# Performance work log

Hardware: AMD Instinct MI355X
Metric: run time of the kernel (lower is better)

The kernel has to match this reference:

```python
import jax, jax.numpy as jnp
import numpy as np

EPS = 1e-20
SCALE = 1.0 / np.sqrt(128.0).astype(np.float32)


def setup_inputs() -> dict:
    key = jax.random.key(0)
    k1, k2 = jax.random.split(key)
    B, K, J, I = 64, 16, 512, 128
    inputs = jax.random.normal(k1, (B, J, I), dtype=jnp.float32)
    W = jax.random.normal(k2, (K, J, I), dtype=jnp.float32)
    b = jnp.zeros((K, J, 1), dtype=jnp.float32)
    return {"inputs": inputs, "W": W, "b": b}


def _squash(s):
    # squash(v) = (1 - 1/(exp(||v||)+eps)) * v / (||v|| + eps), norm over last dim
    n = jnp.linalg.norm(s, axis=-1, keepdims=True)
    return (1.0 - 1.0 / (jnp.exp(n) + EPS)) * (s / (n + EPS))


def reference(inputs, W, b):
    # inputs: (B, J, I); W: (K, J, I); b: (K, J, 1)
    u = inputs[..., None, :, :] * W            # (B, K, J, I) broadcast multiply
    c = jnp.sum(u * u, axis=-1, keepdims=True) * SCALE  # (B, K, J, 1)
    c = jax.nn.softmax(c, axis=0)              # softmax over BATCH dim, as in source
    c = c + b                                  # bias broadcast over batch
    s = jnp.sum(u * c, axis=-2)                # (B, K, I) weighted sum over in_channel
    return _squash(s)
```

## Files before the change

### kernel.cpp

```cpp
#include <hip/hip_runtime.h>
#include <math.h>

#define B 64
#define K 16
#define J 512
#define I 128
#define SCALE 0.08838834764831845f
#define EPSF 1e-20f

typedef __attribute__((ext_vector_type(8))) short short8;
typedef __attribute__((ext_vector_type(4))) float f32x4;

static __device__ __forceinline__ unsigned f2bf(float f) {
    union { float f; unsigned u; } v; v.f = f;
    return (v.u + 0x7FFFu + ((v.u >> 16) & 1u)) >> 16;
}

__global__ __launch_bounds__(64) void k1_mfma(const float* __restrict__ x,
                                              const float* __restrict__ w,
                                              const float* __restrict__ bias,
                                              float* __restrict__ cw) {
    __shared__ __align__(16) char lx[64 * 256];
    __shared__ __align__(16) char lw[16 * 256];

    const int j = blockIdx.x;
    const int l = threadIdx.x;
    const int q = l & 31, hi = l >> 5;

    const float4* xs = (const float4*)x;
    const float4* wsrc = (const float4*)w;

#pragma unroll
    for (int it = 0; it < 32; ++it) {
        int b = it * 2 + hi;
        float4 v = xs[((size_t)b * J + j) * 32 + q];
        uint2 u;
        u.x = f2bf(v.x * v.x) | (f2bf(v.y * v.y) << 16);
        u.y = f2bf(v.z * v.z) | (f2bf(v.w * v.w) << 16);
        *(uint2*)(lx + b * 256 + ((q * 8) ^ ((b & 7) << 4))) = u;
    }
#pragma unroll
    for (int it = 0; it < 8; ++it) {
        int k = it * 2 + hi;
        float4 v = wsrc[((size_t)k * J + j) * 32 + q];
        uint2 u;
        u.x = f2bf(v.x * v.x) | (f2bf(v.y * v.y) << 16);
        u.y = f2bf(v.z * v.z) | (f2bf(v.w * v.w) << 16);
        *(uint2*)(lw + k * 256 + ((q * 8) ^ ((k & 7) << 4))) = u;
    }
    __syncthreads();

    const int g = l >> 4, n = l & 15;
    f32x4 acc[4];
#pragma unroll
    for (int t = 0; t < 4; ++t) acc[t] = (f32x4){0.f, 0.f, 0.f, 0.f};

#pragma unroll
    for (int s = 0; s < 4; ++s) {
        const int colb = s * 64 + g * 16;
        short8 af = *(const short8*)(lw + n * 256 + (colb ^ ((n & 7) << 4)));
#pragma unroll
        for (int t = 0; t < 4; ++t) {
            int row = t * 16 + n;
            short8 bf = *(const short8*)(lx + row * 256 + (colb ^ ((row & 7) << 4)));
            acc[t] = __builtin_amdgcn_mfma_f32_16x16x32_bf16(af, bf, acc[t], 0, 0, 0);
        }
    }

    float sc[4][4];
#pragma unroll
    for (int t = 0; t < 4; ++t)
#pragma unroll
        for (int r = 0; r < 4; ++r) sc[t][r] = acc[t][r] * SCALE;

#pragma unroll
    for (int r = 0; r < 4; ++r) {
        float mx = fmaxf(fmaxf(sc[0][r], sc[1][r]), fmaxf(sc[2][r], sc[3][r]));
#pragma unroll
        for (int msk = 1; msk <= 8; msk <<= 1) mx = fmaxf(mx, __shfl_xor(mx, msk, 64));
        float e0 = expf(sc[0][r] - mx), e1 = expf(sc[1][r] - mx);
        float e2 = expf(sc[2][r] - mx), e3 = expf(sc[3][r] - mx);
        float sum = e0 + e1 + e2 + e3;
#pragma unroll
        for (int msk = 1; msk <= 8; msk <<= 1) sum += __shfl_xor(sum, msk, 64);
        float inv = 1.f / sum;
        int m = g * 4 + r;
        float bi = bias[m * J + j];
        size_t base = ((size_t)m * J + j) * B + n;
        cw[base]      = e0 * inv + bi;
        cw[base + 16] = e1 * inv + bi;
        cw[base + 32] = e2 * inv + bi;
        cw[base + 48] = e3 * inv + bi;
    }
}

__global__ __launch_bounds__(256) void k3_wsum(
    const float* __restrict__ x, const float* __restrict__ w,
    const float* __restrict__ cw, float* __restrict__ sp, int Jc) {
    __shared__ float cl[128 * 16];
    __shared__ float red[256 * 36];

    const int nwg = gridDim.x;
    const int raw = blockIdx.x;
    const int cpx = nwg >> 3;
    const int swz = (raw & 7) * cpx + (raw >> 3);
    const int kt = swz & 3;
    const int bt = (swz >> 2) & 15;
    const int jh = swz >> 6;
    const int j0 = jh * Jc;
    const int b0 = bt * 4, k0 = kt * 4;

    const int iq = threadIdx.x & 31;
    const int js = threadIdx.x >> 5;

    for (int idx = threadIdx.x; idx < Jc * 16; idx += 256) {
        int jj = idx >> 4, kk = (idx >> 2) & 3, bb = idx & 3;
        cl[idx] = cw[((size_t)(k0 + kk) * J + j0 + jj) * B + b0 + bb];
    }
    __syncthreads();

    float4 acc[4][4];
#pragma unroll
    for (int bb = 0; bb < 4; ++bb)
#pragma unroll
        for (int kk = 0; kk < 4; ++kk) acc[bb][kk] = make_float4(0.f, 0.f, 0.f, 0.f);

    for (int j = j0 + js; j < j0 + Jc; j += 8) {
        float4 xv[4], wv[4];
#pragma unroll
        for (int bb = 0; bb < 4; ++bb)
            xv[bb] = *(const float4*)(x + ((size_t)(b0 + bb) * J + j) * I + iq * 4);
#pragma unroll
        for (int kk = 0; kk < 4; ++kk)
            wv[kk] = *(const float4*)(w + ((size_t)(k0 + kk) * J + j) * I + iq * 4);
        const float* cj = cl + (j - j0) * 16;
#pragma unroll
        for (int kk = 0; kk < 4; ++kk) {
#pragma unroll
            for (int bb = 0; bb < 4; ++bb) {
                float c = cj[kk * 4 + bb];
                acc[bb][kk].x = fmaf(xv[bb].x * wv[kk].x, c, acc[bb][kk].x);
                acc[bb][kk].y = fmaf(xv[bb].y * wv[kk].y, c, acc[bb][kk].y);
                acc[bb][kk].z = fmaf(xv[bb].z * wv[kk].z, c, acc[bb][kk].z);
                acc[bb][kk].w = fmaf(xv[bb].w * wv[kk].w, c, acc[bb][kk].w);
            }
        }
    }

#pragma unroll
    for (int r = 0; r < 2; ++r) {
        __syncthreads();
#pragma unroll
        for (int s = 0; s < 8; ++s) {
            int slot = r * 8 + s;
            int bb = slot >> 2, kk = slot & 3;
            *(float4*)(red + (js * 32 + iq) * 36 + s * 4) = acc[bb][kk];
        }
        __syncthreads();
        int iq2 = threadIdx.x & 31, s2 = threadIdx.x >> 5;
        float4 v = make_float4(0.f, 0.f, 0.f, 0.f);
#pragma unroll
        for (int jss = 0; jss < 8; ++jss) {
            float4 u = *(const float4*)(red + (jss * 32 + iq2) * 36 + s2 * 4);
            v.x += u.x; v.y += u.y; v.z += u.z; v.w += u.w;
        }
        int slot = r * 8 + s2;
        int bb = slot >> 2, kk = slot & 3;
        *(float4*)(sp + (((size_t)jh * B + b0 + bb) * K + k0 + kk) * I + iq2 * 4) = v;
    }
}

__global__ __launch_bounds__(128) void k4_squash(const float* __restrict__ sp,
                                                 float* __restrict__ out, int nparts) {
    const int bk = blockIdx.x;
    const int i = threadIdx.x;
    const size_t stride = (size_t)B * K * I;
    const size_t base = (size_t)bk * I + i;

    float s = 0.f;
    for (int p = 0; p < nparts; ++p) s += sp[base + p * stride];

    float q = s * s;
#pragma unroll
    for (int m = 32; m >= 1; m >>= 1) q += __shfl_xor(q, m, 64);
    __shared__ float red2[2];
    if ((threadIdx.x & 63) == 0) red2[threadIdx.x >> 6] = q;
    __syncthreads();
    float nsq = red2[0] + red2[1];

    float n = sqrtf(nsq);
    float factor = (1.0f - 1.0f / (expf(n) + EPSF)) / (n + EPSF);
    out[base] = s * factor;
}

extern "C" void kernel_launch(void* const* d_in, const int* in_sizes, int n_in,
                              void* d_out, int out_size, void* d_ws, size_t ws_size,
                              hipStream_t stream) {
    const float* x    = (const float*)d_in[0];
    const float* w    = (const float*)d_in[1];
    const float* bias = (const float*)d_in[2];
    float* out = (float*)d_out;

    const size_t cwf   = (size_t)K * J * B;
    const size_t partf = (size_t)B * K * I;

    int jc = 16;
    if (ws_size < (cwf + 16 * partf) * 4) jc = 8;
    if (ws_size < (cwf + 8 * partf) * 4)  jc = 4;
    const int Jc = J / jc;

    float* cw = (float*)d_ws;
    float* sp = cw + cwf;

    hipLaunchKernelGGL(k1_mfma,  dim3(J),       dim3(64),  0, stream, x, w, bias, cw);
    hipLaunchKernelGGL(k3_wsum,  dim3(64 * jc), dim3(256), 0, stream, x, w, cw, sp, Jc);
    hipLaunchKernelGGL(k4_squash, dim3(B * K),  dim3(128), 0, stream, sp, out, jc);
}
```

Baseline: 29.84 us.

## Retile capsule kernels: wider k1 loads, tiled weight layout, fixed J split, lighter reductions

```diff
diff --git a/kernel.cpp b/kernel.cpp
--- a/kernel.cpp
+++ b/kernel.cpp
@@ -7,6 +7,8 @@
 #define I 128
 #define SCALE 0.08838834764831845f
 #define EPSF 1e-20f
+#define JC 8
+#define JCW 64
 
 typedef __attribute__((ext_vector_type(8))) short short8;
 typedef __attribute__((ext_vector_type(4))) float f32x4;
@@ -16,41 +18,42 @@
     return (v.u + 0x7FFFu + ((v.u >> 16) & 1u)) >> 16;
 }
 
-__global__ __launch_bounds__(64) void k1_mfma(const float* __restrict__ x,
-                                              const float* __restrict__ w,
-                                              const float* __restrict__ bias,
-                                              float* __restrict__ cw) {
-    __shared__ __align__(16) char lx[64 * 256];
-    __shared__ __align__(16) char lw[16 * 256];
-
-    const int j = blockIdx.x;
-    const int l = threadIdx.x;
-    const int q = l & 31, hi = l >> 5;
-
-    const float4* xs = (const float4*)x;
-    const float4* wsrc = (const float4*)w;
-
-#pragma unroll
-    for (int it = 0; it < 32; ++it) {
-        int b = it * 2 + hi;
-        float4 v = xs[((size_t)b * J + j) * 32 + q];
+__global__ __launch_bounds__(256) void k1_mfma(const float* __restrict__ x,
+                                               const float* __restrict__ w,
+                                               const float* __restrict__ bias,
+                                               float* __restrict__ cw2) {
+    __shared__ __align__(16) char lds[80 * 256];
+    char* lx = lds;
+    char* lw = lds + 64 * 256;
+
+    const int raw = blockIdx.x;
+    const int j = (raw & 7) * JCW + (raw >> 3);
+    const int tid = threadIdx.x;
+
+#pragma unroll
+    for (int r = 0; r < 8; ++r) {
+        int item = tid + 256 * r;
+        int row = item >> 5, q = item & 31;
+        float4 v = *(const float4*)(x + ((size_t)row * J + j) * I + q * 4);
         uint2 u;
         u.x = f2bf(v.x * v.x) | (f2bf(v.y * v.y) << 16);
         u.y = f2bf(v.z * v.z) | (f2bf(v.w * v.w) << 16);
-        *(uint2*)(lx + b * 256 + ((q * 8) ^ ((b & 7) << 4))) = u;
-    }
-#pragma unroll
-    for (int it = 0; it < 8; ++it) {
-        int k = it * 2 + hi;
-        float4 v = wsrc[((size_t)k * J + j) * 32 + q];
+        *(uint2*)(lx + row * 256 + ((q * 8) ^ ((row & 7) << 4))) = u;
+    }
+#pragma unroll
+    for (int r = 0; r < 2; ++r) {
+        int item = tid + 256 * r;
+        int k = item >> 5, q = item & 31;
+        float4 v = *(const float4*)(w + ((size_t)k * J + j) * I + q * 4);
         uint2 u;
         u.x = f2bf(v.x * v.x) | (f2bf(v.y * v.y) << 16);
         u.y = f2bf(v.z * v.z) | (f2bf(v.w * v.w) << 16);
-        *(uint2*)(lw + k * 256 + ((q * 8) ^ ((k & 7) << 4))) = u;
+        *(uint2*)(lw + k * 256 + ((k & 7) ? ((q * 8) ^ ((k & 7) << 4)) : q * 8)) = u;
     }
     __syncthreads();
-
-    const int g = l >> 4, n = l & 15;
+    if (tid >= 64) return;
+
+    const int g = tid >> 4, n = tid & 15;
     f32x4 acc[4];
 #pragma unroll
     for (int t = 0; t < 4; ++t) acc[t] = (f32x4){0.f, 0.f, 0.f, 0.f};
@@ -67,56 +70,47 @@
         }
     }
 
-    float sc[4][4];
-#pragma unroll
-    for (int t = 0; t < 4; ++t)
-#pragma unroll
-        for (int r = 0; r < 4; ++r) sc[t][r] = acc[t][r] * SCALE;
-
 #pragma unroll
     for (int r = 0; r < 4; ++r) {
-        float mx = fmaxf(fmaxf(sc[0][r], sc[1][r]), fmaxf(sc[2][r], sc[3][r]));
+        float s0 = acc[0][r] * SCALE, s1 = acc[1][r] * SCALE;
+        float s2 = acc[2][r] * SCALE, s3 = acc[3][r] * SCALE;
+        float mx = fmaxf(fmaxf(s0, s1), fmaxf(s2, s3));
 #pragma unroll
         for (int msk = 1; msk <= 8; msk <<= 1) mx = fmaxf(mx, __shfl_xor(mx, msk, 64));
-        float e0 = expf(sc[0][r] - mx), e1 = expf(sc[1][r] - mx);
-        float e2 = expf(sc[2][r] - mx), e3 = expf(sc[3][r] - mx);
+        float e0 = expf(s0 - mx), e1 = expf(s1 - mx);
+        float e2 = expf(s2 - mx), e3 = expf(s3 - mx);
         float sum = e0 + e1 + e2 + e3;
 #pragma unroll
         for (int msk = 1; msk <= 8; msk <<= 1) sum += __shfl_xor(sum, msk, 64);
         float inv = 1.f / sum;
         int m = g * 4 + r;
         float bi = bias[m * J + j];
-        size_t base = ((size_t)m * J + j) * B + n;
-        cw[base]      = e0 * inv + bi;
-        cw[base + 16] = e1 * inv + bi;
-        cw[base + 32] = e2 * inv + bi;
-        cw[base + 48] = e3 * inv + bi;
-    }
-}
-
-__global__ __launch_bounds__(256) void k3_wsum(
-    const float* __restrict__ x, const float* __restrict__ w,
-    const float* __restrict__ cw, float* __restrict__ sp, int Jc) {
-    __shared__ float cl[128 * 16];
-    __shared__ float red[256 * 36];
-
-    const int nwg = gridDim.x;
+        size_t base = (size_t)g * 131072 + (size_t)j * 16 + r * 4 + (n & 3);
+        cw2[base + (size_t)(0 * 4 + (n >> 2)) * 8192] = e0 * inv + bi;
+        cw2[base + (size_t)(1 * 4 + (n >> 2)) * 8192] = e1 * inv + bi;
+        cw2[base + (size_t)(2 * 4 + (n >> 2)) * 8192] = e2 * inv + bi;
+        cw2[base + (size_t)(3 * 4 + (n >> 2)) * 8192] = e3 * inv + bi;
+    }
+}
+
+__global__ __launch_bounds__(256) void k3_wsum(const float* __restrict__ x,
+                                               const float* __restrict__ w,
+                                               const float* __restrict__ cw2,
+                                               float* __restrict__ sp) {
+    __shared__ float cl[JCW * 16];
+    __shared__ __align__(16) float4 red[4 * 16 * 32];
+
     const int raw = blockIdx.x;
-    const int cpx = nwg >> 3;
-    const int swz = (raw & 7) * cpx + (raw >> 3);
-    const int kt = swz & 3;
-    const int bt = (swz >> 2) & 15;
-    const int jh = swz >> 6;
-    const int j0 = jh * Jc;
-    const int b0 = bt * 4, k0 = kt * 4;
+    const int swz = (raw & 7) * 64 + (raw >> 3);
+    const int kt = swz & 3, bt = (swz >> 2) & 15, jh = swz >> 6;
+    const int j0 = jh * JCW, b0 = bt * 4, k0 = kt * 4;
 
     const int iq = threadIdx.x & 31;
     const int js = threadIdx.x >> 5;
 
-    for (int idx = threadIdx.x; idx < Jc * 16; idx += 256) {
-        int jj = idx >> 4, kk = (idx >> 2) & 3, bb = idx & 3;
-        cl[idx] = cw[((size_t)(k0 + kk) * J + j0 + jj) * B + b0 + bb];
-    }
+    ((float4*)cl)[threadIdx.x] =
+        ((const float4*)(cw2 + (size_t)kt * 131072 + (size_t)bt * 8192 +
+                         (size_t)j0 * 16))[threadIdx.x];
     __syncthreads();
 
     float4 acc[4][4];
@@ -125,7 +119,9 @@
 #pragma unroll
         for (int kk = 0; kk < 4; ++kk) acc[bb][kk] = make_float4(0.f, 0.f, 0.f, 0.f);
 
-    for (int j = j0 + js; j < j0 + Jc; j += 8) {
+#pragma unroll 2
+    for (int it = 0; it < 8; ++it) {
+        int j = j0 + js + it * 8;
         float4 xv[4], wv[4];
 #pragma unroll
         for (int bb = 0; bb < 4; ++bb)
@@ -133,7 +129,7 @@
 #pragma unroll
         for (int kk = 0; kk < 4; ++kk)
             wv[kk] = *(const float4*)(w + ((size_t)(k0 + kk) * J + j) * I + iq * 4);
-        const float* cj = cl + (j - j0) * 16;
+        const float* cj = cl + (js + it * 8) * 16;
 #pragma unroll
         for (int kk = 0; kk < 4; ++kk) {
 #pragma unroll
@@ -148,49 +144,59 @@
     }
 
 #pragma unroll
-    for (int r = 0; r < 2; ++r) {
-        __syncthreads();
-#pragma unroll
-        for (int s = 0; s < 8; ++s) {
-            int slot = r * 8 + s;
-            int bb = slot >> 2, kk = slot & 3;
-            *(float4*)(red + (js * 32 + iq) * 36 + s * 4) = acc[bb][kk];
+    for (int bb = 0; bb < 4; ++bb)
+#pragma unroll
+        for (int kk = 0; kk < 4; ++kk) {
+            acc[bb][kk].x += __shfl_xor(acc[bb][kk].x, 32, 64);
+            acc[bb][kk].y += __shfl_xor(acc[bb][kk].y, 32, 64);
+            acc[bb][kk].z += __shfl_xor(acc[bb][kk].z, 32, 64);
+            acc[bb][kk].w += __shfl_xor(acc[bb][kk].w, 32, 64);
         }
-        __syncthreads();
-        int iq2 = threadIdx.x & 31, s2 = threadIdx.x >> 5;
-        float4 v = make_float4(0.f, 0.f, 0.f, 0.f);
-#pragma unroll
-        for (int jss = 0; jss < 8; ++jss) {
-            float4 u = *(const float4*)(red + (jss * 32 + iq2) * 36 + s2 * 4);
-            v.x += u.x; v.y += u.y; v.z += u.z; v.w += u.w;
-        }
-        int slot = r * 8 + s2;
+
+    const int wv4 = threadIdx.x >> 6;
+    const int hi = (threadIdx.x >> 5) & 1;
+#pragma unroll
+    for (int r = 0; r < 8; ++r) {
+        int slot = hi * 8 + r;
+        red[(wv4 * 16 + slot) * 32 + iq] = acc[slot >> 2][slot & 3];
+    }
+    __syncthreads();
+
+#pragma unroll
+    for (int rep = 0; rep < 2; ++rep) {
+        int slot = rep * 8 + (threadIdx.x >> 5);
+        float4 a = red[(0 * 16 + slot) * 32 + iq];
+        float4 b = red[(1 * 16 + slot) * 32 + iq];
+        float4 c = red[(2 * 16 + slot) * 32 + iq];
+        float4 d = red[(3 * 16 + slot) * 32 + iq];
+        float4 v = make_float4(a.x + b.x + c.x + d.x, a.y + b.y + c.y + d.y,
+                               a.z + b.z + c.z + d.z, a.w + b.w + c.w + d.w);
         int bb = slot >> 2, kk = slot & 3;
-        *(float4*)(sp + (((size_t)jh * B + b0 + bb) * K + k0 + kk) * I + iq2 * 4) = v;
-    }
-}
-
-__global__ __launch_bounds__(128) void k4_squash(const float* __restrict__ sp,
-                                                 float* __restrict__ out, int nparts) {
-    const int bk = blockIdx.x;
-    const int i = threadIdx.x;
-    const size_t stride = (size_t)B * K * I;
-    const size_t base = (size_t)bk * I + i;
-
-    float s = 0.f;
-    for (int p = 0; p < nparts; ++p) s += sp[base + p * stride];
-
-    float q = s * s;
+        *(float4*)(sp + (((size_t)jh * B + b0 + bb) * K + k0 + kk) * I + iq * 4) = v;
+    }
+}
+
+__global__ __launch_bounds__(256) void k4_squash(const float* __restrict__ sp,
+                                                 float* __restrict__ out) {
+    const int wv = threadIdx.x >> 6;
+    const int lane = threadIdx.x & 63;
+    const int bk = blockIdx.x * 4 + wv;
+    const int b = bk >> 4, k = bk & 15;
+
+    float s0 = 0.f, s1 = 0.f;
+#pragma unroll
+    for (int p = 0; p < JC; ++p) {
+        float2 v = *(const float2*)(sp + (((size_t)p * B + b) * K + k) * I + lane * 2);
+        s0 += v.x; s1 += v.y;
+    }
+    float q = s0 * s0 + s1 * s1;
 #pragma unroll
     for (int m = 32; m >= 1; m >>= 1) q += __shfl_xor(q, m, 64);
-    __shared__ float red2[2];
-    if ((threadIdx.x & 63) == 0) red2[threadIdx.x >> 6] = q;
-    __syncthreads();
-    float nsq = red2[0] + red2[1];
-
-    float n = sqrtf(nsq);
+
+    float n = sqrtf(q);
     float factor = (1.0f - 1.0f / (expf(n) + EPSF)) / (n + EPSF);
-    out[base] = s * factor;
+    float2 o = make_float2(s0 * factor, s1 * factor);
+    *(float2*)(out + ((size_t)b * K + k) * I + lane * 2) = o;
 }
 
 extern "C" void kernel_launch(void* const* d_in, const int* in_sizes, int n_in,
@@ -201,18 +207,10 @@
     const float* bias = (const float*)d_in[2];
     float* out = (float*)d_out;
 
-    const size_t cwf   = (size_t)K * J * B;
-    const size_t partf = (size_t)B * K * I;
-
-    int jc = 16;
-    if (ws_size < (cwf + 16 * partf) * 4) jc = 8;
-    if (ws_size < (cwf + 8 * partf) * 4)  jc = 4;
-    const int Jc = J / jc;
-
-    float* cw = (float*)d_ws;
-    float* sp = cw + cwf;
-
-    hipLaunchKernelGGL(k1_mfma,  dim3(J),       dim3(64),  0, stream, x, w, bias, cw);
-    hipLaunchKernelGGL(k3_wsum,  dim3(64 * jc), dim3(256), 0, stream, x, w, cw, sp, Jc);
-    hipLaunchKernelGGL(k4_squash, dim3(B * K),  dim3(128), 0, stream, sp, out, jc);
-}
+    float* cw2 = (float*)d_ws;
+    float* sp  = cw2 + (size_t)K * J * B;
+
+    hipLaunchKernelGGL(k1_mfma,  dim3(J),   dim3(256), 0, stream, x, w, bias, cw2);
+    hipLaunchKernelGGL(k3_wsum,  dim3(512), dim3(256), 0, stream, x, w, cw2, sp);
+    hipLaunchKernelGGL(k4_squash, dim3(256), dim3(256), 0, stream, sp, out);
+}
```

New measurement: 41.60 us. +39.4%, slower.
